# Optimization experiments

Hardware: AMD Instinct MI355X
Metric: run time of the kernel (lower is better)

The kernel has to match this reference:

```python
import jax, jax.numpy as jnp
import numpy as np

N, D, C = 50000, 128, 64
E = 800000
IN_DIM = 3 * D
EPS = 1e-8
TINY = 1e-12


def _manifold_point(key, n, d, hyperbolic):
    # expmap0 of a random tangent vector at origin o = e0 (ambient dim d)
    v = 0.3 * jax.random.normal(key, (n, d - 1), dtype=jnp.float32)
    nv = jnp.linalg.norm(v, axis=-1, keepdims=True)
    u = v / jnp.maximum(nv, TINY)
    if hyperbolic:  # Lorentz hyperboloid: (cosh|v|, sinh|v| u)
        return jnp.concatenate([jnp.cosh(nv), jnp.sinh(nv) * u], axis=-1)
    else:           # unit sphere: (cos|v|, sin|v| u)
        return jnp.concatenate([jnp.cos(nv), jnp.sin(nv) * u], axis=-1)


def logmap0_lorentz(x):
    # tangent at origin: first coord 0, spatial part = arccosh(x0) * x_r/|x_r|
    x0 = x[..., :1]
    xr = x[..., 1:]
    nr = jnp.linalg.norm(xr, axis=-1, keepdims=True)
    dist = jnp.arccosh(jnp.maximum(x0, 1.0))
    return jnp.concatenate([jnp.zeros_like(x0), dist * xr / jnp.maximum(nr, TINY)], axis=-1)


def logmap0_sphere(x):
    x0 = x[..., :1]
    xr = x[..., 1:]
    nr = jnp.linalg.norm(xr, axis=-1, keepdims=True)
    theta = jnp.arccos(jnp.clip(x0, -1.0, 1.0))
    return jnp.concatenate([jnp.zeros_like(x0), theta * xr / jnp.maximum(nr, TINY)], axis=-1)


def gcn_conv(x, edge_index, W, b, n):
    # PyG GCNConv: add self-loops, symmetric normalization D^-1/2 (A+I) D^-1/2 (X W) + b
    loops = jnp.arange(n, dtype=edge_index.dtype)
    src = jnp.concatenate([edge_index[0], loops])
    dst = jnp.concatenate([edge_index[1], loops])
    deg = jax.ops.segment_sum(jnp.ones_like(dst, dtype=x.dtype), dst, num_segments=n)
    dinv = jnp.where(deg > 0, deg ** -0.5, 0.0)
    norm = dinv[src] * dinv[dst]                 # [E+N]
    h = x @ W                                    # [N, cls_dim]
    msg = h[src] * norm[:, None]                 # [E+N, cls_dim]
    return jax.ops.segment_sum(msg, dst, num_segments=n) + b


def setup_inputs() -> dict:
    key = jax.random.key(0)
    k = jax.random.split(key, 7)
    x_E = jax.random.normal(k[0], (N, D), dtype=jnp.float32)
    x_H = _manifold_point(k[1], N, D, hyperbolic=True)
    x_S = _manifold_point(k[2], N, D, hyperbolic=False)
    edge_index = jax.random.randint(k[3], (2, E), 0, N, dtype=jnp.int64)
    W = jax.random.normal(k[4], (IN_DIM, D), dtype=jnp.float32) / np.sqrt(IN_DIM)
    b = jnp.zeros((D,), dtype=jnp.float32)
    cls_emb = jax.random.normal(k[5], (C, D), dtype=jnp.float32)
    return {"x_E": x_E, "x_H": x_H, "x_S": x_S, "edge_index": edge_index,
            "W": W, "b": b, "cls_emb": cls_emb}


def reference(x_E, x_H, x_S, edge_index, W, b, cls_emb):
    x_h = logmap0_lorentz(x_H)
    x_s = logmap0_sphere(x_S)
    x = jnp.concatenate([x_E, x_h, x_s], axis=-1)          # [N, 3D]
    x = gcn_conv(x, edge_index, W, b, N)                   # [N, D]
    # broadcast cosine similarity (torch eps=1e-8 semantics)
    xn = x / jnp.maximum(jnp.linalg.norm(x, axis=-1, keepdims=True), EPS)
    cn = cls_emb / jnp.maximum(jnp.linalg.norm(cls_emb, axis=-1, keepdims=True), EPS)
    return xn @ cn.T                                       # [N, C]
```

## Files before the change

kernel.cpp:

```cpp
#include <hip/hip_runtime.h>
#include <hip/hip_fp16.h>
#include <math.h>

#define NN 50000
#define DD 128
#define CC 64
#define EE 800000
#define IND 384
#define MAXDEG 64
#define CSTRIDE 16

typedef __attribute__((ext_vector_type(8))) _Float16 h8v;
typedef __attribute__((ext_vector_type(4))) float f4v;

static __device__ __forceinline__ unsigned short f2h(float f) {
  _Float16 h = (_Float16)f;
  return *reinterpret_cast<unsigned short*>(&h);
}
static __device__ __forceinline__ float h2f(unsigned short u) {
  _Float16 h = *reinterpret_cast<_Float16*>(&u);
  return (float)h;
}
static __device__ __forceinline__ float hlo(unsigned int u) {
  return h2f((unsigned short)(u & 0xffffu));
}
static __device__ __forceinline__ float hhi(unsigned int u) {
  return h2f((unsigned short)(u >> 16));
}
static __device__ __forceinline__ h8v hzero() {
  h8v v = {0, 0, 0, 0, 0, 0, 0, 0};
  return v;
}

#define SCAL_B 12500
#define WT_B   192
__global__ __launch_bounds__(256) void k_prep(const float* __restrict__ W,
                                              const float* __restrict__ cls,
                                              const float* __restrict__ xH,
                                              const float* __restrict__ xS,
                                              unsigned short* __restrict__ Wt,
                                              unsigned int* __restrict__ clsp,
                                              float* __restrict__ ch,
                                              float* __restrict__ cs,
                                              int4* __restrict__ cnt4, int n4) {
  int bid = blockIdx.x;
  if (bid < SCAL_B) {
    int gw = bid * 4 + (threadIdx.x >> 6);
    int lane = threadIdx.x & 63;
    const float2* h2 = (const float2*)(xH) + (size_t)gw * 64;
    float2 vh = h2[lane];
    float ssh = vh.x * vh.x + vh.y * vh.y;
    if (lane == 0) ssh -= vh.x * vh.x;
#pragma unroll
    for (int off = 32; off; off >>= 1) ssh += __shfl_down(ssh, off);
    const float2* s2 = (const float2*)(xS) + (size_t)gw * 64;
    float2 vs = s2[lane];
    float sss = vs.x * vs.x + vs.y * vs.y;
    if (lane == 0) sss -= vs.x * vs.x;
#pragma unroll
    for (int off = 32; off; off >>= 1) sss += __shfl_down(sss, off);
    if (lane == 0) {
      float nrh = sqrtf(ssh);
      float dist = acoshf(fmaxf(vh.x, 1.0f));
      ch[gw] = dist / fmaxf(nrh, 1e-12f);
      float nrs = sqrtf(sss);
      float th = acosf(fminf(fmaxf(vs.x, -1.0f), 1.0f));
      cs[gw] = th / fmaxf(nrs, 1e-12f);
    }
  } else if (bid < SCAL_B + WT_B) {
    int flat = (bid - SCAL_B) * 256 + threadIdx.x;
    int n = flat / IND;
    int k = flat - n * IND;
    Wt[(size_t)n * IND + k] = f2h(W[(size_t)k * DD + n]);
  } else if (bid == SCAL_B + WT_B) {
    int wave = threadIdx.x >> 6, lane = threadIdx.x & 63;
    for (int c = wave; c < CC; c += 4) {
      const float2* r2 = (const float2*)(cls + (size_t)c * DD);
      float2 v = r2[lane];
      float ss = v.x * v.x + v.y * v.y;
#pragma unroll
      for (int off = 32; off; off >>= 1) ss += __shfl_xor(ss, off);
      float inv = 1.0f / fmaxf(sqrtf(ss), 1e-8f);
      clsp[c * 64 + lane] =
          (unsigned int)f2h(v.x * inv) | ((unsigned int)f2h(v.y * inv) << 16);
    }
  } else {
    int i = (bid - (SCAL_B + WT_B + 1)) * 256 + threadIdx.x;
    if (i < n4) cnt4[i] = make_int4(0, 0, 0, 0);
  }
}

__global__ __launch_bounds__(256) void k_cplace(const int* __restrict__ src,
                                                const int* __restrict__ dst,
                                                int* __restrict__ cnt,
                                                unsigned short* __restrict__ col2) {
  int e = blockIdx.x * 256 + threadIdx.x;
  if (e >= EE) return;
  int d = dst[e];
  int s = src[e];
  int slot = atomicAdd(&cnt[(size_t)d * CSTRIDE], 1);
  if (slot < MAXDEG) col2[(size_t)d * MAXDEG + slot] = (unsigned short)s;
}

__global__ __launch_bounds__(256) void k_gemm(const float* __restrict__ xE,
                                              const float* __restrict__ xH,
                                              const float* __restrict__ xS,
                                              const int* __restrict__ cnt,
                                              const float* __restrict__ sc1,
                                              const float* __restrict__ sc2,
                                              const unsigned short* __restrict__ Wt,
                                              unsigned short* __restrict__ h) {
  __shared__ unsigned short Ah[32 * 64];
  int tid = threadIdx.x;
  int lane = tid & 63;
  int wid = tid >> 6;
  int c0 = wid * 32;
  int bm0 = blockIdx.x * 32;
  int l15 = lane & 15;
  int lhi = lane >> 4;

  f4v acc[2][2];
#pragma unroll
  for (int m = 0; m < 2; ++m)
#pragma unroll
    for (int nf = 0; nf < 2; ++nf) acc[m][nf] = f4v{0.f, 0.f, 0.f, 0.f};

  for (int kb = 0; kb < IND; kb += 64) {
    int sec = kb >> 7;
    int off = kb & 127;
    const float* __restrict__ src = (sec == 0) ? xE : (sec == 1) ? xH : xS;
#pragma unroll
    for (int it = 0; it < 2; ++it) {
      int flat = tid + it * 256;
      int row = flat >> 4;
      int f4 = flat & 15;
      int node = bm0 + row;
      float4 v = make_float4(0.f, 0.f, 0.f, 0.f);
      float scale = 0.f;
      if (node < NN) {
        v = *(const float4*)&src[(size_t)node * DD + off + f4 * 4];
        float dv = 1.0f / sqrtf((float)(cnt[(size_t)node * CSTRIDE] + 1));
        scale = (sec == 0) ? dv : (sec == 1) ? sc1[node] * dv : sc2[node] * dv;
      }
      v.x *= scale; v.y *= scale; v.z *= scale; v.w *= scale;
      if (sec > 0 && off == 0 && f4 == 0) v.x = 0.f;
      ushort4 o;
      o.x = f2h(v.x); o.y = f2h(v.y); o.z = f2h(v.z); o.w = f2h(v.w);
      int idx = (row * 64 + f4 * 4) ^ ((row & 7) << 3);
      *(ushort4*)&Ah[idx] = o;
    }
    __syncthreads();
#pragma unroll
    for (int ks = 0; ks < 2; ++ks) {
      h8v a[2];
#pragma unroll
      for (int m = 0; m < 2; ++m) {
        int row = m * 16 + l15;
        int idx = (row * 64 + ks * 32 + lhi * 8) ^ ((row & 7) << 3);
        a[m] = *reinterpret_cast<const h8v*>(&Ah[idx]);
      }
      int kk = kb + ks * 32 + lhi * 8;
#pragma unroll
      for (int nf = 0; nf < 2; ++nf) {
        int n = c0 + nf * 16 + l15;
        h8v b = *reinterpret_cast<const h8v*>(&Wt[(size_t)n * IND + kk]);
#pragma unroll
        for (int m = 0; m < 2; ++m)
          acc[m][nf] = __builtin_amdgcn_mfma_f32_16x16x32_f16(a[m], b, acc[m][nf], 0, 0, 0);
      }
    }
    __syncthreads();
  }
#pragma unroll
  for (int m = 0; m < 2; ++m)
#pragma unroll
    for (int nf = 0; nf < 2; ++nf) {
      int colx = c0 + nf * 16 + l15;
      int rowb = bm0 + m * 16 + lhi * 4;
#pragma unroll
      for (int j = 0; j < 4; ++j) {
        int node = rowb + j;
        if (node < NN) h[(size_t)node * DD + colx] = f2h(acc[m][nf][j]);
      }
    }
}

__global__ __launch_bounds__(256) void k_aggn(const unsigned short* __restrict__ h,
                                              const int* __restrict__ cnt,
                                              const unsigned short* __restrict__ col2,
                                              const float* __restrict__ b,
                                              unsigned int* __restrict__ xn) {
  int tid = threadIdx.x;
  int wave = tid >> 6;
  int slot = (tid >> 4) & 3;
  int li = tid & 15;
  int node = blockIdx.x * 16 + wave * 4 + slot;

  const uint4* h4 = (const uint4*)h;
  int rawc = cnt[(size_t)node * CSTRIDE];
  float dv = 1.0f / sqrtf((float)(rawc + 1));
  uint4 hv = h4[(size_t)node * 16 + li];
  float a0 = hlo(hv.x), a1 = hhi(hv.x), a2 = hlo(hv.y), a3 = hhi(hv.y);
  float a4 = hlo(hv.z), a5 = hhi(hv.z), a6 = hlo(hv.w), a7 = hhi(hv.w);
  int ecnt = rawc;
  if (ecnt > MAXDEG) ecnt = MAXDEG;
  const unsigned short* crow = col2 + (size_t)node * MAXDEG;
  int j = 0;
  for (; j + 15 < ecnt; j += 16) {
    int cc[16];
    uint4 vv[16];
#pragma unroll
    for (int q = 0; q < 16; ++q) cc[q] = crow[j + q];
#pragma unroll
    for (int q = 0; q < 16; ++q) vv[q] = h4[(size_t)cc[q] * 16 + li];
#pragma unroll
    for (int q = 0; q < 16; ++q) {
      a0 += hlo(vv[q].x);
      a1 += hhi(vv[q].x);
      a2 += hlo(vv[q].y);
      a3 += hhi(vv[q].y);
      a4 += hlo(vv[q].z);
      a5 += hhi(vv[q].z);
      a6 += hlo(vv[q].w);
      a7 += hhi(vv[q].w);
    }
  }
  for (; j + 3 < ecnt; j += 4) {
    int c0_ = crow[j], c1_ = crow[j + 1], c2_ = crow[j + 2], c3_ = crow[j + 3];
    uint4 v0 = h4[(size_t)c0_ * 16 + li];
    uint4 v1 = h4[(size_t)c1_ * 16 + li];
    uint4 v2 = h4[(size_t)c2_ * 16 + li];
    uint4 v3 = h4[(size_t)c3_ * 16 + li];
    a0 += hlo(v0.x) + hlo(v1.x) + hlo(v2.x) + hlo(v3.x);
    a1 += hhi(v0.x) + hhi(v1.x) + hhi(v2.x) + hhi(v3.x);
    a2 += hlo(v0.y) + hlo(v1.y) + hlo(v2.y) + hlo(v3.y);
    a3 += hhi(v0.y) + hhi(v1.y) + hhi(v2.y) + hhi(v3.y);
    a4 += hlo(v0.z) + hlo(v1.z) + hlo(v2.z) + hlo(v3.z);
    a5 += hhi(v0.z) + hhi(v1.z) + hhi(v2.z) + hhi(v3.z);
    a6 += hlo(v0.w) + hlo(v1.w) + hlo(v2.w) + hlo(v3.w);
    a7 += hhi(v0.w) + hhi(v1.w) + hhi(v2.w) + hhi(v3.w);
  }
  for (; j < ecnt; ++j) {
    uint4 v = h4[(size_t)crow[j] * 16 + li];
    a0 += hlo(v.x);
    a1 += hhi(v.x);
    a2 += hlo(v.y);
    a3 += hhi(v.y);
    a4 += hlo(v.z);
    a5 += hhi(v.z);
    a6 += hlo(v.w);
    a7 += hhi(v.w);
  }
  float4 b0 = ((const float4*)b)[li * 2];
  float4 b1 = ((const float4*)b)[li * 2 + 1];
  float r0 = dv * a0 + b0.x;
  float r1 = dv * a1 + b0.y;
  float r2 = dv * a2 + b0.z;
  float r3 = dv * a3 + b0.w;
  float r4 = dv * a4 + b1.x;
  float r5 = dv * a5 + b1.y;
  float r6 = dv * a6 + b1.z;
  float r7 = dv * a7 + b1.w;
  float ss = r0 * r0 + r1 * r1 + r2 * r2 + r3 * r3 +
             r4 * r4 + r5 * r5 + r6 * r6 + r7 * r7;
#pragma unroll
  for (int off = 8; off; off >>= 1) ss += __shfl_xor(ss, off);
  float inv = 1.0f / fmaxf(sqrtf(ss), 1e-8f);
  uint4 o;
  o.x = (unsigned int)f2h(r0 * inv) | ((unsigned int)f2h(r1 * inv) << 16);
  o.y = (unsigned int)f2h(r2 * inv) | ((unsigned int)f2h(r3 * inv) << 16);
  o.z = (unsigned int)f2h(r4 * inv) | ((unsigned int)f2h(r5 * inv) << 16);
  o.w = (unsigned int)f2h(r6 * inv) | ((unsigned int)f2h(r7 * inv) << 16);
  ((uint4*)xn)[(size_t)node * 16 + li] = o;
}

__global__ __launch_bounds__(256) void k_outg(const unsigned short* __restrict__ xn,
                                              const unsigned short* __restrict__ clsp,
                                              float* __restrict__ out) {
  int tid = threadIdx.x;
  int lane = tid & 63;
  int wid = tid >> 6;
  int l15 = lane & 15, lhi = lane >> 4;
  int bm0 = blockIdx.x * 128 + wid * 32;

  f4v acc[2][4];
#pragma unroll
  for (int m = 0; m < 2; ++m)
#pragma unroll
    for (int nf = 0; nf < 4; ++nf) acc[m][nf] = f4v{0.f, 0.f, 0.f, 0.f};

#pragma unroll
  for (int ks = 0; ks < 4; ++ks) {
    h8v a[2];
#pragma unroll
    for (int m = 0; m < 2; ++m) {
      int row = bm0 + m * 16 + l15;
      a[m] = (row < NN)
                 ? *reinterpret_cast<const h8v*>(&xn[(size_t)row * DD + ks * 32 + lhi * 8])
                 : hzero();
    }
#pragma unroll
    for (int nf = 0; nf < 4; ++nf) {
      int n = nf * 16 + l15;
      h8v b = *reinterpret_cast<const h8v*>(&clsp[(size_t)n * DD + ks * 32 + lhi * 8]);
#pragma unroll
      for (int m = 0; m < 2; ++m)
        acc[m][nf] = __builtin_amdgcn_mfma_f32_16x16x32_f16(a[m], b, acc[m][nf], 0, 0, 0);
    }
  }
#pragma unroll
  for (int m = 0; m < 2; ++m)
#pragma unroll
    for (int nf = 0; nf < 4; ++nf) {
      int colx = nf * 16 + l15;
      int rowb = bm0 + m * 16 + lhi * 4;
#pragma unroll
      for (int j = 0; j < 4; ++j) {
        int row = rowb + j;
        if (row < NN) out[(size_t)row * CC + colx] = acc[m][nf][j];
      }
    }
}

extern "C" void kernel_launch(void* const* d_in, const int* in_sizes, int n_in,
                              void* d_out, int out_size, void* d_ws, size_t ws_size,
                              hipStream_t stream) {
  const float* xE = (const float*)d_in[0];
  const float* xH = (const float*)d_in[1];
  const float* xS = (const float*)d_in[2];
  const int* ei = (const int*)d_in[3];
  const float* W = (const float*)d_in[4];
  const float* b = (const float*)d_in[5];
  const float* cls = (const float*)d_in[6];
  float* out = (float*)d_out;

  char* ws = (char*)d_ws;
  size_t off = 0;
  auto alloc = [&](size_t bytes) {
    void* p = ws + off;
    off = (off + bytes + 255) & ~(size_t)255;
    return p;
  };
  unsigned short* h = (unsigned short*)alloc((size_t)NN * DD * 2);
  unsigned int* xn = (unsigned int*)alloc((size_t)NN * 64 * 4);
  float* chv = (float*)alloc((size_t)NN * 4);
  float* csv = (float*)alloc((size_t)NN * 4);
  int* cnt = (int*)alloc((size_t)NN * CSTRIDE * 4);
  unsigned short* col2 = (unsigned short*)alloc((size_t)NN * MAXDEG * 2);
  unsigned short* Wt = (unsigned short*)alloc((size_t)DD * IND * 2);
  unsigned int* clsp = (unsigned int*)alloc((size_t)CC * 64 * 4);

  const int* esrc = ei;
  const int* edst = ei + EE;
  const int N4 = NN * CSTRIDE / 4;
  const int ZB = (N4 + 255) / 256;

  k_prep<<<SCAL_B + WT_B + 1 + ZB, 256, 0, stream>>>(W, cls, xH, xS, Wt, clsp,
                                                     chv, csv, (int4*)cnt, N4);
  k_cplace<<<(EE + 255) / 256, 256, 0, stream>>>(esrc, edst, cnt, col2);
  k_gemm<<<(NN + 31) / 32, 256, 0, stream>>>(xE, xH, xS, cnt, chv, csv, Wt, h);
  k_aggn<<<(NN + 15) / 16, 256, 0, stream>>>(h, cnt, col2, b, xn);
  k_outg<<<(NN + 127) / 128, 256, 0, stream>>>((const unsigned short*)xn,
                                               (const unsigned short*)clsp, out);
}
```

Baseline: 146.2 us.

## Fuse aggregation with cosine-similarity output GEMM and merge edge placement into prep

```diff
diff --git a/kernel.cpp b/kernel.cpp
--- a/kernel.cpp
+++ b/kernel.cpp
@@ -27,26 +27,51 @@
 static __device__ __forceinline__ float hhi(unsigned int u) {
   return h2f((unsigned short)(u >> 16));
 }
-static __device__ __forceinline__ h8v hzero() {
-  h8v v = {0, 0, 0, 0, 0, 0, 0, 0};
-  return v;
-}
-
+
+__global__ __launch_bounds__(256) void k_zero(int4* __restrict__ cnt4, int n4) {
+  int i = blockIdx.x * 256 + threadIdx.x;
+  if (i < n4) cnt4[i] = make_int4(0, 0, 0, 0);
+}
+
+#define C_B 3125
 #define SCAL_B 12500
-#define WT_B   192
-__global__ __launch_bounds__(256) void k_prep(const float* __restrict__ W,
+#define WT_B 192
+#define P_B (SCAL_B + WT_B + 1)
+#define MEGA_B (C_B + P_B)
+__global__ __launch_bounds__(256) void k_mega(const int* __restrict__ esrc,
+                                              const int* __restrict__ edst,
+                                              int* __restrict__ cnt,
+                                              unsigned short* __restrict__ col2,
+                                              const float* __restrict__ W,
                                               const float* __restrict__ cls,
                                               const float* __restrict__ xH,
                                               const float* __restrict__ xS,
                                               unsigned short* __restrict__ Wt,
                                               unsigned int* __restrict__ clsp,
                                               float* __restrict__ ch,
-                                              float* __restrict__ cs,
-                                              int4* __restrict__ cnt4, int n4) {
+                                              float* __restrict__ cs) {
   int bid = blockIdx.x;
-  if (bid < SCAL_B) {
-    int gw = bid * 4 + (threadIdx.x >> 6);
-    int lane = threadIdx.x & 63;
+  int tid = threadIdx.x;
+  int cid = -1, pid = -1;
+  if (bid < 5 * C_B) {
+    if (bid % 5 == 0) cid = bid / 5;
+    else pid = bid - bid / 5 - 1;
+  } else {
+    pid = bid - C_B;
+  }
+
+  if (cid >= 0) {
+    int e = cid * 256 + tid;
+    int d = edst[e];
+    int s = esrc[e];
+    int slot = atomicAdd(&cnt[(size_t)d * CSTRIDE], 1);
+    if (slot < MAXDEG) col2[(size_t)d * MAXDEG + slot] = (unsigned short)s;
+    return;
+  }
+
+  if (pid < SCAL_B) {
+    int gw = pid * 4 + (tid >> 6);
+    int lane = tid & 63;
     const float2* h2 = (const float2*)(xH) + (size_t)gw * 64;
     float2 vh = h2[lane];
     float ssh = vh.x * vh.x + vh.y * vh.y;
@@ -67,13 +92,13 @@
       float th = acosf(fminf(fmaxf(vs.x, -1.0f), 1.0f));
       cs[gw] = th / fmaxf(nrs, 1e-12f);
     }
-  } else if (bid < SCAL_B + WT_B) {
-    int flat = (bid - SCAL_B) * 256 + threadIdx.x;
+  } else if (pid < SCAL_B + WT_B) {
+    int flat = (pid - SCAL_B) * 256 + tid;
     int n = flat / IND;
     int k = flat - n * IND;
     Wt[(size_t)n * IND + k] = f2h(W[(size_t)k * DD + n]);
-  } else if (bid == SCAL_B + WT_B) {
-    int wave = threadIdx.x >> 6, lane = threadIdx.x & 63;
+  } else {
+    int wave = tid >> 6, lane = tid & 63;
     for (int c = wave; c < CC; c += 4) {
       const float2* r2 = (const float2*)(cls + (size_t)c * DD);
       float2 v = r2[lane];
@@ -84,22 +109,7 @@
       clsp[c * 64 + lane] =
           (unsigned int)f2h(v.x * inv) | ((unsigned int)f2h(v.y * inv) << 16);
     }
-  } else {
-    int i = (bid - (SCAL_B + WT_B + 1)) * 256 + threadIdx.x;
-    if (i < n4) cnt4[i] = make_int4(0, 0, 0, 0);
-  }
-}
-
-__global__ __launch_bounds__(256) void k_cplace(const int* __restrict__ src,
-                                                const int* __restrict__ dst,
-                                                int* __restrict__ cnt,
-                                                unsigned short* __restrict__ col2) {
-  int e = blockIdx.x * 256 + threadIdx.x;
-  if (e >= EE) return;
-  int d = dst[e];
-  int s = src[e];
-  int slot = atomicAdd(&cnt[(size_t)d * CSTRIDE], 1);
-  if (slot < MAXDEG) col2[(size_t)d * MAXDEG + slot] = (unsigned short)s;
+  }
 }
 
 __global__ __launch_bounds__(256) void k_gemm(const float* __restrict__ xE,
@@ -185,16 +195,17 @@
     }
 }
 
-__global__ __launch_bounds__(256) void k_aggn(const unsigned short* __restrict__ h,
-                                              const int* __restrict__ cnt,
-                                              const unsigned short* __restrict__ col2,
-                                              const float* __restrict__ b,
-                                              unsigned int* __restrict__ xn) {
+__global__ __launch_bounds__(256) void k_aggout(const unsigned short* __restrict__ h,
+                                                const int* __restrict__ cnt,
+                                                const unsigned short* __restrict__ col2,
+                                                const float* __restrict__ b,
+                                                const unsigned int* __restrict__ clsp,
+                                                float* __restrict__ out) {
+  __shared__ unsigned int xl[16 * 64];
   int tid = threadIdx.x;
-  int wave = tid >> 6;
-  int slot = (tid >> 4) & 3;
   int li = tid & 15;
-  int node = blockIdx.x * 16 + wave * 4 + slot;
+  int node16 = tid >> 4;
+  int node = blockIdx.x * 16 + node16;
 
   const uint4* h4 = (const uint4*)h;
   int rawc = cnt[(size_t)node * CSTRIDE];
@@ -271,55 +282,29 @@
   o.y = (unsigned int)f2h(r2 * inv) | ((unsigned int)f2h(r3 * inv) << 16);
   o.z = (unsigned int)f2h(r4 * inv) | ((unsigned int)f2h(r5 * inv) << 16);
   o.w = (unsigned int)f2h(r6 * inv) | ((unsigned int)f2h(r7 * inv) << 16);
-  ((uint4*)xn)[(size_t)node * 16 + li] = o;
-}
-
-__global__ __launch_bounds__(256) void k_outg(const unsigned short* __restrict__ xn,
-                                              const unsigned short* __restrict__ clsp,
-                                              float* __restrict__ out) {
-  int tid = threadIdx.x;
+  int widx = (node16 * 64 + li * 4) ^ ((node16 & 7) << 2);
+  *(uint4*)&xl[widx] = o;
+  __syncthreads();
+
   int lane = tid & 63;
   int wid = tid >> 6;
   int l15 = lane & 15, lhi = lane >> 4;
-  int bm0 = blockIdx.x * 128 + wid * 32;
-
-  f4v acc[2][4];
-#pragma unroll
-  for (int m = 0; m < 2; ++m)
-#pragma unroll
-    for (int nf = 0; nf < 4; ++nf) acc[m][nf] = f4v{0.f, 0.f, 0.f, 0.f};
-
+  f4v acc = f4v{0.f, 0.f, 0.f, 0.f};
+  const uint4* clsp4 = (const uint4*)clsp;
 #pragma unroll
   for (int ks = 0; ks < 4; ++ks) {
-    h8v a[2];
-#pragma unroll
-    for (int m = 0; m < 2; ++m) {
-      int row = bm0 + m * 16 + l15;
-      a[m] = (row < NN)
-                 ? *reinterpret_cast<const h8v*>(&xn[(size_t)row * DD + ks * 32 + lhi * 8])
-                 : hzero();
-    }
-#pragma unroll
-    for (int nf = 0; nf < 4; ++nf) {
-      int n = nf * 16 + l15;
-      h8v b = *reinterpret_cast<const h8v*>(&clsp[(size_t)n * DD + ks * 32 + lhi * 8]);
-#pragma unroll
-      for (int m = 0; m < 2; ++m)
-        acc[m][nf] = __builtin_amdgcn_mfma_f32_16x16x32_f16(a[m], b, acc[m][nf], 0, 0, 0);
-    }
-  }
-#pragma unroll
-  for (int m = 0; m < 2; ++m)
-#pragma unroll
-    for (int nf = 0; nf < 4; ++nf) {
-      int colx = nf * 16 + l15;
-      int rowb = bm0 + m * 16 + lhi * 4;
-#pragma unroll
-      for (int j = 0; j < 4; ++j) {
-        int row = rowb + j;
-        if (row < NN) out[(size_t)row * CC + colx] = acc[m][nf][j];
-      }
-    }
+    int ridx = (l15 * 64 + ks * 16 + lhi * 4) ^ ((l15 & 7) << 2);
+    h8v a = *reinterpret_cast<const h8v*>(&xl[ridx]);
+    int n = wid * 16 + l15;
+    uint4 bq = clsp4[n * 16 + ks * 4 + lhi];
+    h8v bb = *reinterpret_cast<const h8v*>(&bq);
+    acc = __builtin_amdgcn_mfma_f32_16x16x32_f16(a, bb, acc, 0, 0, 0);
+  }
+#pragma unroll
+  for (int j2 = 0; j2 < 4; ++j2) {
+    int nodeo = blockIdx.x * 16 + lhi * 4 + j2;
+    out[(size_t)nodeo * CC + wid * 16 + l15] = acc[j2];
+  }
 }
 
 extern "C" void kernel_launch(void* const* d_in, const int* in_sizes, int n_in,
@@ -342,7 +327,6 @@
     return p;
   };
   unsigned short* h = (unsigned short*)alloc((size_t)NN * DD * 2);
-  unsigned int* xn = (unsigned int*)alloc((size_t)NN * 64 * 4);
   float* chv = (float*)alloc((size_t)NN * 4);
   float* csv = (float*)alloc((size_t)NN * 4);
   int* cnt = (int*)alloc((size_t)NN * CSTRIDE * 4);
@@ -353,13 +337,10 @@
   const int* esrc = ei;
   const int* edst = ei + EE;
   const int N4 = NN * CSTRIDE / 4;
-  const int ZB = (N4 + 255) / 256;
-
-  k_prep<<<SCAL_B + WT_B + 1 + ZB, 256, 0, stream>>>(W, cls, xH, xS, Wt, clsp,
-                                                     chv, csv, (int4*)cnt, N4);
-  k_cplace<<<(EE + 255) / 256, 256, 0, stream>>>(esrc, edst, cnt, col2);
+
+  k_zero<<<(N4 + 255) / 256, 256, 0, stream>>>((int4*)cnt, N4);
+  k_mega<<<MEGA_B, 256, 0, stream>>>(esrc, edst, cnt, col2, W, cls, xH, xS,
+                                     Wt, clsp, chv, csv);
   k_gemm<<<(NN + 31) / 32, 256, 0, stream>>>(xE, xH, xS, cnt, chv, csv, Wt, h);
-  k_aggn<<<(NN + 15) / 16, 256, 0, stream>>>(h, cnt, col2, b, xn);
-  k_outg<<<(NN + 127) / 128, 256, 0, stream>>>((const unsigned short*)xn,
-                                               (const unsigned short*)clsp, out);
-}
+  k_aggout<<<NN / 16, 256, 0, stream>>>(h, cnt, col2, b, clsp, out);
+}
```

Measured after the change: 122.8 us, median of 2. 1.19x faster.
